# Kernel tuning notes

Hardware: AMD Instinct MI355X
Metric: run time of the kernel (lower is better)

## Reference

```python
import jax, jax.numpy as jnp
import numpy as np

D_MODEL = 1024
NUM_HEADS = 16
HEAD_DIM = D_MODEL // NUM_HEADS
MAX_SEQ_LEN = 2048
THETA = 10000.0
B, T = 2, 2048


def precompute_cos_sin(head_dim, max_len, theta):
    freqs = 1.0 / theta ** (jnp.arange(0, head_dim, 2, dtype=jnp.float32) / head_dim)
    t = jnp.arange(max_len, dtype=jnp.float32)
    f = jnp.outer(t, freqs)  # [max_len, head_dim//2]
    return jnp.concatenate([jnp.cos(f), jnp.sin(f)], axis=-1)  # [max_len, head_dim]


def apply_rotary_emb(x, cos_sin):
    # x: [B, H, T, Hs]; cos_sin: [T, Hs]
    xr = x.reshape(*x.shape[:-1], -1, 2)
    x1, x2 = xr[..., 0], xr[..., 1]
    cos, sin = jnp.split(cos_sin, 2, axis=-1)  # each [T, Hs//2]
    out = jnp.stack([x1 * cos - x2 * sin, x1 * sin + x2 * cos], axis=-1)
    return out.reshape(x.shape).astype(x.dtype)


def setup_inputs() -> dict:
    key = jax.random.key(0)
    ks = jax.random.split(key, 5)
    scale = 1.0 / np.sqrt(D_MODEL)
    return {
        'x': jax.random.normal(ks[0], (B, T, D_MODEL), dtype=jnp.float32),
        'wq': jax.random.normal(ks[1], (D_MODEL, D_MODEL), dtype=jnp.float32) * scale,
        'wk': jax.random.normal(ks[2], (D_MODEL, D_MODEL), dtype=jnp.float32) * scale,
        'wv': jax.random.normal(ks[3], (D_MODEL, D_MODEL), dtype=jnp.float32) * scale,
        'wo': jax.random.normal(ks[4], (D_MODEL, D_MODEL), dtype=jnp.float32) * scale,
    }


def reference(x, wq, wk, wv, wo):
    seq_len = x.shape[1]
    # Linear: einsum('...i,oi->...o'), weight stored as [out, in]
    q = jnp.einsum('bti,oi->bto', x, wq)
    k = jnp.einsum('bti,oi->bto', x, wk)
    v = jnp.einsum('bti,oi->bto', x, wv)
    # split heads: B T (nH Hs) -> B nH T Hs
    def split_heads(t):
        return t.reshape(t.shape[0], t.shape[1], NUM_HEADS, HEAD_DIM).transpose(0, 2, 1, 3)
    xq, xk, xv = split_heads(q), split_heads(k), split_heads(v)
    cos_sin = precompute_cos_sin(HEAD_DIM, MAX_SEQ_LEN, THETA)[:seq_len]
    xq = apply_rotary_emb(xq, cos_sin)
    xk = apply_rotary_emb(xk, cos_sin)
    scores = jnp.einsum('bhqd,bhkd->bhqk', xq, xk) / jnp.sqrt(jnp.float32(HEAD_DIM))
    causal = jnp.tril(jnp.ones((seq_len, seq_len), dtype=bool))
    scores = jnp.where(causal[None, None], scores, -jnp.inf)
    attn = jax.nn.softmax(scores, axis=-1)
    xo = jnp.einsum('bhqk,bhkd->bhqd', attn, xv)
    xo = xo.transpose(0, 2, 1, 3).reshape(x.shape[0], seq_len, D_MODEL)
    return jnp.einsum('bti,oi->bto', xo, wo)
```

## Files before the change

### kernel.cpp

```cpp
#include <hip/hip_runtime.h>
#include <hip/hip_bf16.h>

typedef __hip_bfloat16 bf16;
using s8v = __attribute__((ext_vector_type(8))) short;
using s4v = __attribute__((ext_vector_type(4))) short;
using f4v = __attribute__((ext_vector_type(4))) float;
using f16v = __attribute__((ext_vector_type(16))) float;

#define D_MODEL 1024
#define NHEADS  16
#define HDIM    64
#define TSEQ    2048
#define NBATCH  2
#define BT      (NBATCH * TSEQ)

#define QSCALE  0.180336880111f
#define SBIAS  -17.3123404907f

__device__ inline short f2bf_bits(float f) {
    bf16 h = __float2bfloat16(f);
    return *reinterpret_cast<short*>(&h);
}

__device__ inline unsigned cvt_pk_bf16(float lo, float hi) {
    unsigned r;
    asm("v_cvt_pk_bf16_f32 %0, %1, %2" : "=v"(r) : "v"(lo), "v"(hi));
    return r;
}

__device__ inline void perm_swap(unsigned &a, unsigned &b) {
    asm volatile("v_permlane32_swap_b32 %0, %1" : "+v"(a), "+v"(b));
}

__device__ inline void load8(const bf16* p, s8v& o) { o = *(const s8v*)p; }
__device__ inline void load8(const float* p, s8v& o) {
    const f4v a = *(const f4v*)p;
    const f4v b = *(const f4v*)(p + 4);
    s8v r;
    r[0] = f2bf_bits(a[0]); r[1] = f2bf_bits(a[1]);
    r[2] = f2bf_bits(a[2]); r[3] = f2bf_bits(a[3]);
    r[4] = f2bf_bits(b[0]); r[5] = f2bf_bits(b[1]);
    r[6] = f2bf_bits(b[2]); r[7] = f2bf_bits(b[3]);
    o = r;
}

__device__ inline void storeC(bf16* p, float v)  { *p = __float2bfloat16(v); }
__device__ inline void storeC(float* p, float v) { *p = v; }

__device__ inline void gload_lds16(const bf16* g, short* l) {
    __builtin_amdgcn_global_load_lds(
        (__attribute__((address_space(1))) void*)(unsigned long long)(size_t)g,
        (__attribute__((address_space(3))) void*)l,
        16, 0, 0);
}

__device__ inline void stage8(const bf16* g, short* l) { gload_lds16(g, l); }
__device__ inline void stage8(const float* g, short* l) {
    s8v v; load8(g, v); *(s8v*)l = v;
}

__global__ __launch_bounds__(256) void cvt_kernel(
    const float* __restrict__ src, bf16* __restrict__ dst)
{
    const size_t i = ((size_t)blockIdx.x * 256 + threadIdx.x) * 8;
    s8v v; load8(src + i, v);
    *(s8v*)&dst[i] = v;
}

__global__ __launch_bounds__(256) void cvt_all_kernel(
    const float* __restrict__ x,  bf16* __restrict__ xb,
    const float* __restrict__ wq, bf16* __restrict__ wqb,
    const float* __restrict__ wk, bf16* __restrict__ wkb,
    const float* __restrict__ wv, bf16* __restrict__ wvb,
    const float* __restrict__ wo, bf16* __restrict__ wob,
    float2* __restrict__ cs_table)
{
    const int blk = blockIdx.x;
    if (blk >= 4096) {
        const int idx = (blk - 4096) * 256 + threadIdx.x;
        const int tt = idx >> 5;
        const int i  = idx & 31;
        const float inv_freq = expf(-(float)i * (9.210340371976184f / 32.0f));
        float s, c;
        sincosf((float)tt * inv_freq, &s, &c);
        cs_table[idx] = make_float2(c, s);
        return;
    }
    const float* src; bf16* dst; int base;
    if (blk < 2048)      { src = x;  dst = xb;  base = 0; }
    else if (blk < 2560) { src = wq; dst = wqb; base = 2048; }
    else if (blk < 3072) { src = wk; dst = wkb; base = 2560; }
    else if (blk < 3584) { src = wv; dst = wvb; base = 3072; }
    else                 { src = wo; dst = wob; base = 3584; }
    const size_t i = ((size_t)(blk - base) * 256 + threadIdx.x) * 8;
    s8v v; load8(src + i, v);
    *(s8v*)&dst[i] = v;
}

template <int TM, bool ROPE, typename TA, typename TW, typename TC>
__global__ __launch_bounds__(256, 2) void gemm_bt(
    const TA* __restrict__ A,
    const TW* __restrict__ W0, const TW* __restrict__ W1, const TW* __restrict__ W2,
    TC* __restrict__ C0, TC* __restrict__ C1, TC* __restrict__ C2,
    bf16* __restrict__ VT, const float2* __restrict__ cs_table)
{
    const TW* W = (blockIdx.z == 0) ? W0 : (blockIdx.z == 1) ? W1 : W2;
    TC*       C = (blockIdx.z == 0) ? C0 : (blockIdx.z == 1) ? C1 : C2;
    const bool vt_mode = (VT != nullptr) && (blockIdx.z == 2);

    constexpr int K = 1024, N = 1024;
    constexpr int MT = TM / 32;
    __shared__ __align__(16) short As[TM * 64];
    __shared__ __align__(16) short Ws[128 * 64];

    const int t    = threadIdx.x;
    const int lane = t & 63;
    const int wave = t >> 6;
    const int m16  = lane & 15;
    const int quad = lane >> 4;
    const int wm   = (wave >> 1) * (TM / 2);
    const int wn   = (wave & 1) * 64;
    const int rowBase = blockIdx.x * TM;
    const int colBase = blockIdx.y * 128;

    f4v acc[MT][4];
#pragma unroll
    for (int i = 0; i < MT; ++i)
#pragma unroll
        for (int j = 0; j < 4; ++j) acc[i][j] = f4v{0.f, 0.f, 0.f, 0.f};

    for (int kk = 0; kk < K / 64; ++kk) {
#pragma unroll
        for (int r = 0; r < TM / 32; ++r) {
            const int chunk = r * 256 + t;
            const int row   = chunk >> 3;
            const int c8s   = (chunk & 7) ^ (row & 7);
            stage8(A + (size_t)(rowBase + row) * K + kk * 64 + c8s * 8, &As[chunk * 8]);
        }
#pragma unroll
        for (int r = 0; r < 4; ++r) {
            const int chunk = r * 256 + t;
            const int row   = chunk >> 3;
            const int c8s   = (chunk & 7) ^ (row & 7);
            stage8(W + (size_t)(colBase + row) * K + kk * 64 + c8s * 8, &Ws[chunk * 8]);
        }
        __syncthreads();

#pragma unroll
        for (int ks = 0; ks < 2; ++ks) {
            s8v af[MT], bw[4];
#pragma unroll
            for (int mt = 0; mt < MT; ++mt) {
                const int rowa = wm + mt * 16 + m16;
                af[mt] = *(const s8v*)&As[rowa * 64 + ((ks * 4 + quad) ^ (rowa & 7)) * 8];
            }
#pragma unroll
            for (int nt = 0; nt < 4; ++nt) {
                const int roww = wn + nt * 16 + m16;
                bw[nt] = *(const s8v*)&Ws[roww * 64 + ((ks * 4 + quad) ^ (roww & 7)) * 8];
            }
#pragma unroll
            for (int mt = 0; mt < MT; ++mt)
#pragma unroll
                for (int nt = 0; nt < 4; ++nt)
                    acc[mt][nt] = __builtin_amdgcn_mfma_f32_16x16x32_bf16(
                        af[mt], bw[nt], acc[mt][nt], 0, 0, 0);
        }
        __syncthreads();
    }

    if (vt_mode) {
#pragma unroll
        for (int mt = 0; mt < MT; ++mt)
#pragma unroll
            for (int nt = 0; nt < 4; ++nt) {
                const int col  = colBase + wn + nt * 16 + m16;
                const int row0 = rowBase + wm + mt * 16 + quad * 4;
                const int bb   = row0 >> 11;
                const int tt   = row0 & (TSEQ - 1);
                s4v pk;
#pragma unroll
                for (int r = 0; r < 4; ++r) pk[r] = f2bf_bits(acc[mt][nt][r]);
                *(s4v*)&VT[((size_t)(bb * 1024 + col)) * TSEQ + tt] = pk;
            }
    } else {
        const float qs = (ROPE && blockIdx.z == 0) ? QSCALE : 1.0f;
#pragma unroll
        for (int mt = 0; mt < MT; ++mt)
#pragma unroll
            for (int nt = 0; nt < 4; ++nt) {
                const int col = colBase + wn + nt * 16 + m16;
#pragma unroll
                for (int r = 0; r < 4; ++r) {
                    const int row = rowBase + wm + mt * 16 + quad * 4 + r;
                    float v = acc[mt][nt][r];
                    if (ROPE) {
                        const float prt = __shfl_xor(v, 1, 64);
                        const int   tt  = row & (TSEQ - 1);
                        const int   i   = (col & 63) >> 1;
                        const float2 cs = cs_table[tt * 32 + i];
                        v = (col & 1) ? (prt * cs.y + v * cs.x)
                                      : (v * cs.x - prt * cs.y);
                        v *= qs;
                    }
                    storeC(&C[(size_t)row * N + col], v);
                }
            }
    }
}

__global__ __launch_bounds__(256) void rope_inplace(
    bf16* __restrict__ qp, bf16* __restrict__ kp)
{
    const int idx = blockIdx.x * 256 + threadIdx.x;
    const int i  = idx & 31;
    const int h  = (idx >> 5) & (NHEADS - 1);
    const int tt = (idx >> 9) & (TSEQ - 1);
    const int b  = idx >> 20;

    const size_t src = (size_t)(b * TSEQ + tt) * D_MODEL + h * HDIM + 2 * i;

    const float inv_freq = expf(-(float)i * (9.210340371976184f / 32.0f));
    const float f = (float)tt * inv_freq;
    float s, c;
    sincosf(f, &s, &c);

    const float q1 = __bfloat162float(qp[src]);
    const float q2 = __bfloat162float(qp[src + 1]);
    qp[src]     = __float2bfloat16((q1 * c - q2 * s) * QSCALE);
    qp[src + 1] = __float2bfloat16((q1 * s + q2 * c) * QSCALE);

    const float k1 = __bfloat162float(kp[src]);
    const float k2 = __bfloat162float(kp[src + 1]);
    kp[src]     = __float2bfloat16(k1 * c - k2 * s);
    kp[src + 1] = __float2bfloat16(k1 * s + k2 * c);
}

__global__ __launch_bounds__(512, 4) void attn_kernel(
    bf16* __restrict__ qp, const bf16* __restrict__ kp,
    const bf16* __restrict__ vt)
{
    const int hb = blockIdx.x & 31;
    const int bx = 15 - (blockIdx.x >> 5);
    const int h  = hb & (NHEADS - 1);
    const int b  = hb >> 4;
    const int t    = threadIdx.x;
    const int lane = t & 63;
    const int wave = t >> 6;
    const int l31  = lane & 31;
    const int hi   = lane >> 5;
    const int wq   = wave >> 1;
    const int wk   = wave & 1;

    bf16*       Qb  = qp + (size_t)b * TSEQ * D_MODEL + h * HDIM;
    const bf16* Kb  = kp + (size_t)b * TSEQ * D_MODEL + h * HDIM;
    const bf16* Vtb = vt + ((size_t)b * 1024 + h * HDIM) * TSEQ;

    __shared__ __align__(16) short Klds[2][128 * 64];
    __shared__ __align__(16) short Vlds[2][64 * 128];

    auto stage_kv = [&](int buf, int kv0) {
#pragma unroll
        for (int r = 0; r < 2; ++r) {
            const int chunk = r * 512 + t;
            const int row   = chunk >> 3;
            const int c8s   = (chunk & 7) ^ (row & 7);
            gload_lds16(Kb + (size_t)(kv0 + row) * D_MODEL + c8s * 8,
                        &Klds[buf][chunk * 8]);
        }
#pragma unroll
        for (int r = 0; r < 2; ++r) {
            const int chunk = r * 512 + t;
            const int row   = chunk >> 4;
            const int c16s  = (chunk & 15) ^ (row & 15);
            gload_lds16(Vtb + (size_t)row * TSEQ + kv0 + c16s * 8,
                        &Vlds[buf][chunk * 8]);
        }
    };

    const int q0   = bx * 128;
    const int qrow = q0 + wq * 32 + l31;

    const bf16* qptr = Qb + (size_t)qrow * D_MODEL;
    s8v qf[4];
#pragma unroll
    for (int s2 = 0; s2 < 4; ++s2)
        qf[s2] = *(const s8v*)&qptr[s2 * 16 + hi * 8];

    f16v o_acc[2];
#pragma unroll
    for (int db = 0; db < 2; ++db)
#pragma unroll
        for (int r = 0; r < 16; ++r) o_acc[db][r] = 0.0f;
    float l_acc = 0.0f;

    const int iters = bx + 1;

    stage_kv(0, 0);

#pragma unroll 1
    for (int it = 0; it < iters; ++it) {
        const int cur = it & 1;
        const int kv0 = it * 128;

        if (it + 1 < iters) {
            stage_kv(cur ^ 1, kv0 + 128);
            asm volatile("s_waitcnt vmcnt(4)" ::: "memory");
        } else {
            asm volatile("s_waitcnt vmcnt(0)" ::: "memory");
        }
        __builtin_amdgcn_s_barrier();
        __builtin_amdgcn_sched_barrier(0);

        const bool diag = (it == iters - 1);

#pragma unroll
        for (int kb = 0; kb < 2; ++kb) {
            const int rowk = wk * 64 + kb * 32 + l31;
            const short* kbase = &Klds[cur][rowk * 64];
            const int r7 = rowk & 7;
            f16v sacc;
#pragma unroll
            for (int r = 0; r < 16; ++r) sacc[r] = SBIAS;
            __builtin_amdgcn_s_setprio(1);
#pragma unroll
            for (int s2 = 0; s2 < 4; ++s2) {
                const s8v ak = *(const s8v*)&kbase[((s2 * 2 + hi) ^ r7) * 8];
                sacc = __builtin_amdgcn_mfma_f32_32x32x16_bf16(
                    ak, qf[s2], sacc, 0, 0, 0);
            }
            __builtin_amdgcn_s_setprio(0);

#pragma unroll
            for (int r = 0; r < 16; ++r) {
                float p = __builtin_amdgcn_exp2f(sacc[r]);
                if (diag) {
                    const int kg = kv0 + wk * 64 + kb * 32
                                 + (r & 3) + 8 * (r >> 2) + 4 * hi;
                    p = (kg <= qrow) ? p : 0.0f;
                }
                sacc[r] = p;
                l_acc += p;
            }

            __builtin_amdgcn_s_setprio(1);
#pragma unroll
            for (int sh = 0; sh < 2; ++sh) {
                const int h8 = sh * 8;
                unsigned w0 = cvt_pk_bf16(sacc[h8 + 0], sacc[h8 + 1]);
                unsigned w1 = cvt_pk_bf16(sacc[h8 + 2], sacc[h8 + 3]);
                unsigned w2 = cvt_pk_bf16(sacc[h8 + 4], sacc[h8 + 5]);
                unsigned w3 = cvt_pk_bf16(sacc[h8 + 6], sacc[h8 + 7]);
                perm_swap(w0, w2);
                perm_swap(w1, w3);
                union { unsigned u[4]; s8v v; } pu;
                pu.u[0] = w0; pu.u[1] = w1; pu.u[2] = w2; pu.u[3] = w3;
                const int gch = wk * 8 + (kb * 2 + sh) * 2 + hi;
#pragma unroll
                for (int db = 0; db < 2; ++db) {
                    const int rowd = db * 32 + l31;
                    const s8v bv = *(const s8v*)&Vlds[cur][rowd * 128
                                                    + (gch ^ (rowd & 15)) * 8];
                    o_acc[db] = __builtin_amdgcn_mfma_f32_32x32x16_bf16(
                        pu.v, bv, o_acc[db], 0, 0, 0);
                }
            }
            __builtin_amdgcn_s_setprio(0);
        }

        asm volatile("s_waitcnt lgkmcnt(0)" ::: "memory");
        __builtin_amdgcn_s_barrier();
    }

    const float lw = l_acc + __shfl_xor(l_acc, 32, 64);
    float* Xf = (float*)&Klds[0][0];
    float* Lf = (float*)&Vlds[0][0];
    __syncthreads();

    {
        const f16v* opw = (wk == 0) ? &o_acc[1] : &o_acc[0];
#pragma unroll
        for (int r = 0; r < 16; ++r) {
            const int qo = (r & 3) + 8 * (r >> 2) + 4 * hi;
            Xf[((wq * 2 + wk) * 32 + qo) * 32 + l31] = (*opw)[r];
        }
    }
    if (lane < 32) Lf[(wq * 2 + wk) * 32 + l31] = lw;
    __syncthreads();

    {
        const f16v* opm = (wk == 0) ? &o_acc[0] : &o_acc[1];
#pragma unroll
        for (int rg = 0; rg < 4; ++rg) {
            const f4v lp0 = *(const f4v*)&Lf[(wq * 2 + 0) * 32 + rg * 8 + hi * 4];
            const f4v lp1 = *(const f4v*)&Lf[(wq * 2 + 1) * 32 + rg * 8 + hi * 4];
#pragma unroll
            for (int j = 0; j < 4; ++j) {
                const int r  = rg * 4 + j;
                const int qo = rg * 8 + hi * 4 + j;
                const float oo = (*opm)[r]
                    + Xf[((wq * 2 + (1 - wk)) * 32 + qo) * 32 + l31];
                Qb[(size_t)(q0 + wq * 32 + qo) * D_MODEL + wk * 32 + l31] =
                    __float2bfloat16(oo / (lp0[j] + lp1[j]));
            }
        }
    }
}

extern "C" void kernel_launch(void* const* d_in, const int* in_sizes, int n_in,
                              void* d_out, int out_size, void* d_ws, size_t ws_size,
                              hipStream_t stream) {
    const float* x  = (const float*)d_in[0];
    const float* wq = (const float*)d_in[1];
    const float* wk = (const float*)d_in[2];
    const float* wv = (const float*)d_in[3];
    const float* wo = (const float*)d_in[4];
    float* out = (float*)d_out;

    bf16* ws = (bf16*)d_ws;
    const size_t SZ  = (size_t)BT * D_MODEL;
    const size_t SZW = (size_t)D_MODEL * D_MODEL;
    bf16* qp  = ws + 0 * SZ;
    bf16* kp  = ws + 1 * SZ;
    bf16* vt  = (bf16*)d_out;
    bf16* xb  = (bf16*)(out + 2 * 1024 * 1024);

    const size_t need_w    = (2 * SZ + 4 * SZW) * sizeof(bf16);
    const size_t need_full = need_w + 65536 * sizeof(float2);

    if (ws_size >= need_full) {
        bf16*   wqb = ws + 2 * SZ + 0 * SZW;
        bf16*   wkb = ws + 2 * SZ + 1 * SZW;
        bf16*   wvb = ws + 2 * SZ + 2 * SZW;
        bf16*   wob = ws + 2 * SZ + 3 * SZW;
        float2* cst = (float2*)(ws + 2 * SZ + 4 * SZW);

        cvt_all_kernel<<<dim3(4352), 256, 0, stream>>>(
            x, xb, wq, wqb, wk, wkb, wv, wvb, wo, wob, cst);
        gemm_bt<128, true, bf16, bf16, bf16><<<dim3(32, 8, 3), 256, 0, stream>>>(
            xb, wqb, wkb, wvb, qp, kp, qp , vt, cst);
        attn_kernel<<<dim3(512), 512, 0, stream>>>(qp, kp, vt);
        gemm_bt<64, false, bf16, bf16, float><<<dim3(64, 8, 1), 256, 0, stream>>>(
            qp, wob, wob, wob, out, out, out, nullptr, nullptr);
    } else if (ws_size >= need_w) {
        bf16* wqb = ws + 2 * SZ + 0 * SZW;
        bf16* wkb = ws + 2 * SZ + 1 * SZW;
        bf16* wvb = ws + 2 * SZ + 2 * SZW;
        bf16* wob = ws + 2 * SZ + 3 * SZW;
        cvt_all_kernel<<<dim3(4096), 256, 0, stream>>>(
            x, xb, wq, wqb, wk, wkb, wv, wvb, wo, wob, nullptr);
        gemm_bt<128, false, bf16, bf16, bf16><<<dim3(32, 8, 3), 256, 0, stream>>>(
            xb, wqb, wkb, wvb, qp, kp, qp , vt, nullptr);
        rope_inplace<<<dim3(8192), 256, 0, stream>>>(qp, kp);
        attn_kernel<<<dim3(512), 512, 0, stream>>>(qp, kp, vt);
        gemm_bt<64, false, bf16, bf16, float><<<dim3(64, 8, 1), 256, 0, stream>>>(
            qp, wob, wob, wob, out, out, out, nullptr, nullptr);
    } else {
        bf16* wob = kp;
        cvt_kernel<<<dim3(2048), 256, 0, stream>>>(x, xb);
        gemm_bt<128, false, bf16, float, bf16><<<dim3(32, 8, 3), 256, 0, stream>>>(
            xb, wq, wk, wv, qp, kp, qp , vt, nullptr);
        rope_inplace<<<dim3(8192), 256, 0, stream>>>(qp, kp);
        attn_kernel<<<dim3(512), 512, 0, stream>>>(qp, kp, vt);
        cvt_kernel<<<dim3(512), 256, 0, stream>>>(wo, wob);
        gemm_bt<64, false, bf16, bf16, float><<<dim3(64, 8, 1), 256, 0, stream>>>(
            qp, wob, wob, wob, out, out, out, nullptr, nullptr);
    }
}
```

Before: 170.4 us.

## Replace QKV projection GEMM with 256x256-tile double-buffered direct-to-LDS kernel

New measurement: 181.6 us. +6.6%, slower.

```diff
diff --git a/kernel.cpp b/kernel.cpp
--- a/kernel.cpp
+++ b/kernel.cpp
@@ -97,6 +97,156 @@
     *(s8v*)&dst[i] = v;
 }
 
+template <bool ROPE>
+__global__ __launch_bounds__(512, 2) void gemm256(
+    const bf16* __restrict__ A,
+    const bf16* __restrict__ W0, const bf16* __restrict__ W1,
+    const bf16* __restrict__ W2,
+    bf16* __restrict__ C0, bf16* __restrict__ C1,
+    bf16* __restrict__ VT, const float2* __restrict__ cs_table)
+{
+    const bf16* W = (blockIdx.z == 0) ? W0 : (blockIdx.z == 1) ? W1 : W2;
+    bf16*       C = (blockIdx.z == 0) ? C0 : C1;
+    const bool vt_mode = (blockIdx.z == 2);
+
+    constexpr int K = 1024;
+    constexpr int NT = K / 64;
+
+    __shared__ __align__(16) short Alds[2][256 * 64];
+    __shared__ __align__(16) short Blds[2][256 * 64];
+
+    const int t    = threadIdx.x;
+    const int lane = t & 63;
+    const int wave = t >> 6;
+    const int l31  = lane & 31;
+    const int hi   = lane >> 5;
+    const int wm   = (wave >> 2) * 128;
+    const int wn   = (wave & 3) * 64;
+    const int rowBase = blockIdx.x * 256;
+    const int colBase = blockIdx.y * 256;
+
+    auto stage = [&](int buf, int kt) {
+#pragma unroll
+        for (int r = 0; r < 4; ++r) {
+            const int chunk = r * 512 + t;
+            const int row   = chunk >> 3;
+            const int c8    = (chunk & 7) ^ (row & 7);
+            gload_lds16(A + (size_t)(rowBase + row) * K + kt * 64 + c8 * 8,
+                        &Alds[buf][chunk * 8]);
+        }
+#pragma unroll
+        for (int r = 0; r < 4; ++r) {
+            const int chunk = r * 512 + t;
+            const int row   = chunk >> 3;
+            const int c8    = (chunk & 7) ^ (row & 7);
+            gload_lds16(W + (size_t)(colBase + row) * K + kt * 64 + c8 * 8,
+                        &Blds[buf][chunk * 8]);
+        }
+    };
+
+    f16v acc[4][2];
+#pragma unroll
+    for (int mr = 0; mr < 4; ++mr)
+#pragma unroll
+        for (int nr = 0; nr < 2; ++nr)
+#pragma unroll
+            for (int r = 0; r < 16; ++r) acc[mr][nr][r] = 0.0f;
+
+    stage(0, 0);
+
+#pragma unroll 1
+    for (int kt = 0; kt < NT; ++kt) {
+        const int cur = kt & 1;
+
+        if (kt + 1 < NT) {
+            stage(cur ^ 1, kt + 1);
+            asm volatile("s_waitcnt vmcnt(8)" ::: "memory");
+        } else {
+            asm volatile("s_waitcnt vmcnt(0)" ::: "memory");
+        }
+        __builtin_amdgcn_s_barrier();
+        __builtin_amdgcn_sched_barrier(0);
+
+        s8v bf[2][4];
+#pragma unroll
+        for (int nr = 0; nr < 2; ++nr) {
+            const int rowb = wn + nr * 32 + l31;
+            const short* bb_ = &Blds[cur][rowb * 64];
+            const int r7 = rowb & 7;
+#pragma unroll
+            for (int ks = 0; ks < 4; ++ks)
+                bf[nr][ks] = *(const s8v*)&bb_[((ks * 2 + hi) ^ r7) * 8];
+        }
+
+#pragma unroll
+        for (int mr = 0; mr < 4; ++mr) {
+            const int rowa = wm + mr * 32 + l31;
+            const short* ab_ = &Alds[cur][rowa * 64];
+            const int r7 = rowa & 7;
+            s8v af[4];
+#pragma unroll
+            for (int ks = 0; ks < 4; ++ks)
+                af[ks] = *(const s8v*)&ab_[((ks * 2 + hi) ^ r7) * 8];
+            __builtin_amdgcn_s_setprio(1);
+#pragma unroll
+            for (int ks = 0; ks < 4; ++ks) {
+                acc[mr][0] = __builtin_amdgcn_mfma_f32_32x32x16_bf16(
+                    af[ks], bf[0][ks], acc[mr][0], 0, 0, 0);
+                acc[mr][1] = __builtin_amdgcn_mfma_f32_32x32x16_bf16(
+                    af[ks], bf[1][ks], acc[mr][1], 0, 0, 0);
+            }
+            __builtin_amdgcn_s_setprio(0);
+        }
+
+        asm volatile("s_waitcnt lgkmcnt(0)" ::: "memory");
+        __builtin_amdgcn_s_barrier();
+    }
+
+    if (vt_mode) {
+#pragma unroll
+        for (int mr = 0; mr < 4; ++mr)
+#pragma unroll
+            for (int nr = 0; nr < 2; ++nr) {
+                const int col = colBase + wn + nr * 32 + l31;
+#pragma unroll
+                for (int rg = 0; rg < 4; ++rg) {
+                    const int row0 = rowBase + wm + mr * 32 + 8 * rg + 4 * hi;
+                    const int bb2  = row0 >> 11;
+                    const int tt   = row0 & (TSEQ - 1);
+                    s4v pk;
+#pragma unroll
+                    for (int j = 0; j < 4; ++j)
+                        pk[j] = f2bf_bits(acc[mr][nr][rg * 4 + j]);
+                    *(s4v*)&VT[((size_t)(bb2 * 1024 + col)) * TSEQ + tt] = pk;
+                }
+            }
+    } else {
+        const float qs = (ROPE && blockIdx.z == 0) ? QSCALE : 1.0f;
+#pragma unroll
+        for (int mr = 0; mr < 4; ++mr)
+#pragma unroll
+            for (int nr = 0; nr < 2; ++nr) {
+                const int col = colBase + wn + nr * 32 + l31;
+#pragma unroll
+                for (int r = 0; r < 16; ++r) {
+                    const int row = rowBase + wm + mr * 32
+                                  + (r & 3) + 8 * (r >> 2) + 4 * hi;
+                    float v = acc[mr][nr][r];
+                    if (ROPE) {
+                        const float prt = __shfl_xor(v, 1, 64);
+                        const int   tt  = row & (TSEQ - 1);
+                        const int   i   = (col & 63) >> 1;
+                        const float2 cs = cs_table[tt * 32 + i];
+                        v = (col & 1) ? (prt * cs.y + v * cs.x)
+                                      : (v * cs.x - prt * cs.y);
+                        v *= qs;
+                    }
+                    C[(size_t)row * 1024 + col] = __float2bfloat16(v);
+                }
+            }
+    }
+}
+
 template <int TM, bool ROPE, typename TA, typename TW, typename TC>
 __global__ __launch_bounds__(256, 2) void gemm_bt(
     const TA* __restrict__ A,
@@ -437,8 +587,8 @@
 
         cvt_all_kernel<<<dim3(4352), 256, 0, stream>>>(
             x, xb, wq, wqb, wk, wkb, wv, wvb, wo, wob, cst);
-        gemm_bt<128, true, bf16, bf16, bf16><<<dim3(32, 8, 3), 256, 0, stream>>>(
-            xb, wqb, wkb, wvb, qp, kp, qp , vt, cst);
+        gemm256<true><<<dim3(16, 4, 3), 512, 0, stream>>>(
+            xb, wqb, wkb, wvb, qp, kp, vt, cst);
         attn_kernel<<<dim3(512), 512, 0, stream>>>(qp, kp, vt);
         gemm_bt<64, false, bf16, bf16, float><<<dim3(64, 8, 1), 256, 0, stream>>>(
             qp, wob, wob, wob, out, out, out, nullptr, nullptr);
@@ -449,8 +599,8 @@
         bf16* wob = ws + 2 * SZ + 3 * SZW;
         cvt_all_kernel<<<dim3(4096), 256, 0, stream>>>(
             x, xb, wq, wqb, wk, wkb, wv, wvb, wo, wob, nullptr);
-        gemm_bt<128, false, bf16, bf16, bf16><<<dim3(32, 8, 3), 256, 0, stream>>>(
-            xb, wqb, wkb, wvb, qp, kp, qp , vt, nullptr);
+        gemm256<false><<<dim3(16, 4, 3), 512, 0, stream>>>(
+            xb, wqb, wkb, wvb, qp, kp, vt, nullptr);
         rope_inplace<<<dim3(8192), 256, 0, stream>>>(qp, kp);
         attn_kernel<<<dim3(512), 512, 0, stream>>>(qp, kp, vt);
         gemm_bt<64, false, bf16, bf16, float><<<dim3(64, 8, 1), 256, 0, stream>>>(
```
